# Kernel tuning notes

Hardware: AMD Instinct MI355X
Metric: run time of the kernel (lower is better)

The kernel has to match this reference:

```python
import jax, jax.numpy as jnp
import numpy as np

B, S, D, H, FF = 4, 2048, 512, 8, 2048
HD = D // H
SCALE = float(D) ** 0.5  # original scales by sqrt(embed_dim), not sqrt(head_dim)
EPS = 1e-5


def setup_inputs() -> dict:
    key = jax.random.key(0)
    ks = jax.random.split(key, 16)
    s_in = 1.0 / np.sqrt(D)
    s_ff = 1.0 / np.sqrt(FF)
    return {
        "embeddings": jax.random.normal(ks[0], (B, S, D), dtype=jnp.float32),
        "mask": jnp.ones((B, S), dtype=bool),
        # per-head Q/K/V projections stacked: [H, D, HD]
        "Wq": jax.random.uniform(ks[1], (H, D, HD), jnp.float32, -s_in, s_in),
        "bq": jax.random.uniform(ks[2], (H, HD), jnp.float32, -s_in, s_in),
        "Wk": jax.random.uniform(ks[3], (H, D, HD), jnp.float32, -s_in, s_in),
        "bk": jax.random.uniform(ks[4], (H, HD), jnp.float32, -s_in, s_in),
        "Wv": jax.random.uniform(ks[5], (H, D, HD), jnp.float32, -s_in, s_in),
        "bv": jax.random.uniform(ks[6], (H, HD), jnp.float32, -s_in, s_in),
        "Wc": jax.random.uniform(ks[7], (D, D), jnp.float32, -s_in, s_in),
        "bc": jax.random.uniform(ks[8], (D,), jnp.float32, -s_in, s_in),
        "W1": jax.random.uniform(ks[9], (D, FF), jnp.float32, -s_in, s_in),
        "b1": jax.random.uniform(ks[10], (FF,), jnp.float32, -s_in, s_in),
        "W2": jax.random.uniform(ks[11], (FF, D), jnp.float32, -s_ff, s_ff),
        "b2": jax.random.uniform(ks[12], (D,), jnp.float32, -s_ff, s_ff),
        "gamma": jnp.ones((D,), jnp.float32),
        "beta": jnp.zeros((D,), jnp.float32),
    }


def reference(embeddings, mask, Wq, bq, Wk, bk, Wv, bv, Wc, bc, W1, b1, W2, b2, gamma, beta):
    # Per-head projections batched into one einsum each: [B,H,S,HD]
    Q = jnp.einsum("bsd,hdf->bhsf", embeddings, Wq) + bq[:, None, :]
    K = jnp.einsum("bsd,hdf->bhsf", embeddings, Wk) + bk[:, None, :]
    V = jnp.einsum("bsd,hdf->bhsf", embeddings, Wv) + bv[:, None, :]
    # NOTE: the original computes a masked score tensor but then softmaxes the
    # UNMASKED scores (bug). We faithfully ignore the mask here.
    scores = jnp.einsum("bhsf,bhtf->bhst", Q, K) / SCALE  # [B,H,S,S]
    A = jax.nn.softmax(scores, axis=-1)
    Hh = jnp.einsum("bhst,bhtf->bhsf", A, V)  # [B,H,S,HD]
    # concat heads along feature dim (head h -> contiguous slice)
    Hcat = jnp.transpose(Hh, (0, 2, 1, 3)).reshape(B, S, D)
    Hp = Hcat @ Wc + bc
    # add & norm (dropout is identity at eval)
    res = Hp + embeddings
    mu = jnp.mean(res, axis=-1, keepdims=True)
    var = jnp.var(res, axis=-1, keepdims=True)
    Hn = (res - mu) / jnp.sqrt(var + EPS) * gamma + beta
    out = jax.nn.relu(Hn @ W1 + b1) @ W2 + b2  # no residual after FFN in original
    return out, mask
```

## Files before the change

### kernel.cpp

```cpp
#include <hip/hip_runtime.h>
#include <hip/hip_bf16.h>
#include <cstdint>
#include <cstddef>

typedef short  s16x8 __attribute__((ext_vector_type(8)));
typedef short  s16x4 __attribute__((ext_vector_type(4)));
typedef float  f32x4 __attribute__((ext_vector_type(4)));
typedef unsigned u32x2 __attribute__((ext_vector_type(2)));

static constexpr int Bb = 4, Ss = 2048, Dd = 512, Hh = 8, HDd = 64, FFf = 2048;
static constexpr int Mm = Bb * Ss;

__device__ __forceinline__ unsigned short f2bf(float f) {
  unsigned u = __float_as_uint(f);
  u += 0x7FFFu + ((u >> 16) & 1u);
  return (unsigned short)(u >> 16);
}

__device__ __forceinline__ unsigned cvt_pk_bf16(float lo, float hi) {
  unsigned r;
  asm("v_cvt_pk_bf16_f32 %0, %1, %2" : "=v"(r) : "v"(lo), "v"(hi));
  return r;
}

__device__ __forceinline__ float exp2_raw(float x) {
  float r;
  asm("v_exp_f32 %0, %1\n\ts_nop 0" : "=v"(r) : "v"(x));
  return r;
}

#define GLOAD_LDS16(gp, lp)                                                     \
  __builtin_amdgcn_global_load_lds((const __attribute__((address_space(1))) void*)(gp), \
                                   (__attribute__((address_space(3))) void*)(lp), 16, 0, 0)

__device__ __forceinline__ void xpose_tile(const float* __restrict__ in,
                                           unsigned short* __restrict__ out,
                                           int K, int N, int bx, int by, float (*t)[33]) {
  const int lx = threadIdx.x & 31, ly = threadIdx.x >> 5;
  const int n0 = bx * 32, k0 = by * 32;
#pragma unroll
  for (int r = 0; r < 4; ++r) t[ly + r * 8][lx] = in[(size_t)(k0 + ly + r * 8) * N + n0 + lx];
  __syncthreads();
#pragma unroll
  for (int r = 0; r < 4; ++r)
    out[(size_t)(n0 + ly + r * 8) * K + k0 + lx] = f2bf(t[lx][ly + r * 8]);
}

__global__ __launch_bounds__(256) void prep_all(
    const float* __restrict__ emb, const float* __restrict__ Wq, const float* __restrict__ Wk,
    const float* __restrict__ Wv, const float* __restrict__ Wc, const float* __restrict__ W1,
    const float* __restrict__ W2, unsigned short* __restrict__ embB,
    unsigned short* __restrict__ WtQKV, unsigned short* __restrict__ WtC,
    unsigned short* __restrict__ Wt1, unsigned short* __restrict__ Wt2,
    float* __restrict__ maskOut) {
  __shared__ float t[32][33];
  const int blk = blockIdx.x;
  if (blk < 4096) {
    const int i = blk * 256 + threadIdx.x;
    const float4 v = reinterpret_cast<const float4*>(emb)[i];
    s16x4 o; o[0] = f2bf(v.x); o[1] = f2bf(v.y); o[2] = f2bf(v.z); o[3] = f2bf(v.w);
    reinterpret_cast<s16x4*>(embB)[i] = o;
  } else if (blk < 4864) {
    const int b = blk - 4096;
    const int bx = b & 15, by = (b >> 4) & 1, z = b >> 5;
    const int sel = z >> 3, h = z & 7;
    const float* W = sel == 0 ? Wq : (sel == 1 ? Wk : Wv);
    const float* inb = W + (size_t)h * 512 * 64;
    unsigned short* outb = WtQKV + (size_t)sel * 512 * 512 + (size_t)h * 64 * 512;
    const int lx = threadIdx.x & 31, ly = threadIdx.x >> 5;
    const int d0 = bx * 32, f0 = by * 32;
#pragma unroll
    for (int r = 0; r < 4; ++r) t[ly + r * 8][lx] = inb[(size_t)(d0 + ly + r * 8) * 64 + f0 + lx];
    __syncthreads();
#pragma unroll
    for (int r = 0; r < 4; ++r)
      outb[(size_t)(f0 + ly + r * 8) * 512 + d0 + lx] = f2bf(t[lx][ly + r * 8]);
  } else if (blk < 5120) {
    const int b = blk - 4864;
    xpose_tile(Wc, WtC, 512, 512, b & 15, b >> 4, t);
  } else if (blk < 6144) {
    const int b = blk - 5120;
    xpose_tile(W1, Wt1, 512, 2048, b & 63, b >> 6, t);
  } else if (blk < 7168) {
    const int b = blk - 6144;
    xpose_tile(W2, Wt2, 2048, 512, b & 15, b >> 4, t);
  } else {
    const int i = (blk - 7168) * 256 + threadIdx.x;
    if (i < Bb * Ss) maskOut[i] = 1.0f;
  }
}

__global__ __launch_bounds__(256) void vtrans(const unsigned short* __restrict__ Vn,
                                              unsigned short* __restrict__ Vt) {
  __shared__ unsigned short t[64][72];
  const int bh = blockIdx.y, s0 = blockIdx.x * 64;
  const int row = threadIdx.x >> 2, cs = (threadIdx.x & 3) << 4;
  const unsigned short* src = Vn + (((size_t)bh * 2048 + s0 + row) << 6) + cs;
  *reinterpret_cast<s16x8*>(&t[row][cs]) = *reinterpret_cast<const s16x8*>(src);
  *reinterpret_cast<s16x8*>(&t[row][cs + 8]) = *reinterpret_cast<const s16x8*>(src + 8);
  __syncthreads();
  unsigned ow[8];
#pragma unroll
  for (int j = 0; j < 8; ++j)
    ow[j] = (unsigned)t[cs + 2 * j][row] | ((unsigned)t[cs + 2 * j + 1][row] << 16);
  unsigned short* dst = Vt + (((size_t)bh * 64 + row) << 11) + s0 + cs;
  *reinterpret_cast<uint4*>(dst) = *reinterpret_cast<const uint4*>(&ow[0]);
  *reinterpret_cast<uint4*>(dst + 8) = *reinterpret_cast<const uint4*>(&ow[4]);
}

template<int EPI, int NI>
__global__ __launch_bounds__(256) void gemm_bt(
    const unsigned short* __restrict__ A, const unsigned short* __restrict__ Bt,
    const float* __restrict__ bias0, const float* __restrict__ bias1, const float* __restrict__ bias2,
    const float* __restrict__ addf, float* __restrict__ outF,
    unsigned short* __restrict__ outB0, unsigned short* __restrict__ outB1,
    unsigned short* __restrict__ outB2, int M, int N, int K) {
  constexpr int BN = NI * 32;
  __shared__ alignas(16) unsigned short As[3][128 * 32];
  __shared__ alignas(16) unsigned short Bs[3][BN * 32];
  const int tid = threadIdx.x;
  const int lane = tid & 63, wid = tid >> 6;
  const int wr = wid >> 1, wc = wid & 1;
  const int fr = lane & 15, kg = lane >> 4;
  const int m0 = blockIdx.y * 128, n0 = blockIdx.x * BN;

  const int srow = tid >> 2;
  const int schunk = (tid & 3) ^ ((tid >> 3) & 3);
  const unsigned short* gA = A + (size_t)(m0 + srow) * K + (schunk << 3);
  const unsigned short* gB = Bt + (size_t)(n0 + srow) * K + (schunk << 3);

  auto STAGE = [&](int kt, int buf) {
    unsigned short* lA = &As[buf][wid * 512];
    unsigned short* lB = &Bs[buf][wid * 512];
    GLOAD_LDS16(gA + kt, lA);
    GLOAD_LDS16(gA + (size_t)64 * K + kt, lA + 2048);
    GLOAD_LDS16(gB + kt, lB);
    if constexpr (NI == 4) GLOAD_LDS16(gB + (size_t)64 * K + kt, lB + 2048);
  };

  f32x4 acc[4][NI];
#pragma unroll
  for (int i = 0; i < 4; ++i)
#pragma unroll
    for (int j = 0; j < NI; ++j)
#pragma unroll
      for (int r = 0; r < 4; ++r) acc[i][j][r] = 0.f;

  STAGE(0, 0);
  STAGE(32, 1);
  const int nk = K >> 5;
  int cur = 0;
  const int rchunk = (kg ^ ((fr >> 1) & 3)) << 3;
  for (int ki = 0; ki < nk; ++ki) {
    const int pre = cur == 0 ? 2 : cur - 1;
    __builtin_amdgcn_s_barrier();
    if (ki + 2 < nk) {
      STAGE((ki + 2) << 5, pre);
      if constexpr (NI == 4)
        asm volatile("s_waitcnt vmcnt(8)" ::: "memory");
      else
        asm volatile("s_waitcnt vmcnt(6)" ::: "memory");
    } else if (ki + 1 < nk) {
      if constexpr (NI == 4)
        asm volatile("s_waitcnt vmcnt(4)" ::: "memory");
      else
        asm volatile("s_waitcnt vmcnt(3)" ::: "memory");
    } else {
      asm volatile("s_waitcnt vmcnt(0)" ::: "memory");
    }
    __builtin_amdgcn_sched_barrier(0);
    __builtin_amdgcn_s_barrier();
    __builtin_amdgcn_sched_barrier(0);

    s16x8 af[4], bfv[NI];
#pragma unroll
    for (int i = 0; i < 4; ++i)
      af[i] = *reinterpret_cast<const s16x8*>(&As[cur][(wr * 64 + i * 16 + fr) * 32 + rchunk]);
#pragma unroll
    for (int i = 0; i < NI; ++i)
      bfv[i] = *reinterpret_cast<const s16x8*>(
          &Bs[cur][(wc * (NI * 16) + i * 16 + fr) * 32 + rchunk]);
    __builtin_amdgcn_s_setprio(1);
#pragma unroll
    for (int mi = 0; mi < 4; ++mi)
#pragma unroll
      for (int ni = 0; ni < NI; ++ni)
        acc[mi][ni] = __builtin_amdgcn_mfma_f32_16x16x32_bf16(af[mi], bfv[ni], acc[mi][ni], 0, 0, 0);
    __builtin_amdgcn_s_setprio(0);
    cur = cur == 2 ? 0 : cur + 1;
  }

#pragma unroll
  for (int mi = 0; mi < 4; ++mi)
#pragma unroll
    for (int ni = 0; ni < NI; ++ni)
#pragma unroll
      for (int r = 0; r < 4; ++r) {
        const int row = m0 + wr * 64 + mi * 16 + kg * 4 + r;
        const int col = n0 + wc * (NI * 16) + ni * 16 + fr;
        float v = acc[mi][ni][r];
        if constexpr (EPI == 0) {
          const int sel = col >> 9, c = col & 511;
          const float* bs = sel == 0 ? bias0 : (sel == 1 ? bias1 : bias2);
          v += bs[c];
          const int b = row >> 11, s = row & 2047;
          const int h = c >> 6, f = c & 63;
          unsigned short* ob = sel == 0 ? outB0 : (sel == 1 ? outB1 : outB2);
          ob[((size_t)((b << 3) + h) * 2048 + s) * 64 + f] = f2bf(v);
        } else if constexpr (EPI == 1) {
          const size_t idx = (size_t)row * 512 + col;
          outF[idx] = v + bias0[col] + addf[idx];
        } else if constexpr (EPI == 2) {
          v += bias0[col];
          outB0[(size_t)row * 2048 + col] = f2bf(v > 0.f ? v : 0.f);
        } else {
          outF[(size_t)row * 512 + col] = v + bias0[col];
        }
      }
}

__global__ __launch_bounds__(256) void attn_kernel(const unsigned short* __restrict__ Q,
                                                   const unsigned short* __restrict__ Kx,
                                                   const unsigned short* __restrict__ V,
                                                   unsigned short* __restrict__ Hcat) {
  const int lane = threadIdx.x & 63, wid = threadIdx.x >> 6;
  const int fr = lane & 15, kg = lane >> 4;
  const int lin = blockIdx.x;
  const int xcd = lin & 7, idx = lin >> 3;
  const int bh = xcd * 4 + (idx & 3);
  const int qi = idx >> 2;
  const int b = bh >> 3, h = bh & 7;
  const int q0 = qi * 64 + wid * 16;
  const unsigned short* Qh = Q + (size_t)bh * Ss * HDd;
  const unsigned short* Kh = Kx + (size_t)bh * Ss * HDd;
  const unsigned short* Vh = V + (size_t)bh * HDd * Ss;

  __shared__ alignas(16) unsigned short Ks[2][64 * 64];
  __shared__ alignas(16) unsigned short Vs[64 * 64];
  __shared__ alignas(16) unsigned short P[4][16][72];

  const int srow = lane >> 3;
  const int scol = ((lane & 7) ^ srow) << 3;
  const unsigned short* gK0 = Kh + (size_t)(8 * (2 * wid + 0) + srow) * 64 + scol;
  const unsigned short* gK1 = Kh + (size_t)(8 * (2 * wid + 1) + srow) * 64 + scol;
  const unsigned short* gV0 = Vh + (size_t)(8 * (2 * wid + 0) + srow) * 2048 + scol;
  const unsigned short* gV1 = Vh + (size_t)(8 * (2 * wid + 1) + srow) * 2048 + scol;
  unsigned short* lK0a = &Ks[0][(2 * wid + 0) * 512];
  unsigned short* lK1a = &Ks[0][(2 * wid + 1) * 512];
  unsigned short* lK0b = &Ks[1][(2 * wid + 0) * 512];
  unsigned short* lK1b = &Ks[1][(2 * wid + 1) * 512];
  unsigned short* lV0 = &Vs[(2 * wid + 0) * 512];
  unsigned short* lV1 = &Vs[(2 * wid + 1) * 512];

  s16x8 bq[2];
#pragma unroll
  for (int kb = 0; kb < 2; ++kb)
    bq[kb] = *reinterpret_cast<const s16x8*>(&Qh[(size_t)(q0 + fr) * 64 + kb * 32 + kg * 8]);

  f32x4 o[4];
#pragma unroll
  for (int ct = 0; ct < 4; ++ct)
#pragma unroll
    for (int r = 0; r < 4; ++r) o[ct][r] = 0.f;
  float mr = -1e30f, lsum = 0.f;

  const float iscL = 1.4426950408889634f * 0.044194173824159216f;
  const int swz = (fr & 7) << 3;

  GLOAD_LDS16(gK0, lK0a);
  GLOAD_LDS16(gK1, lK1a);
  GLOAD_LDS16(gV0, lV0);
  GLOAD_LDS16(gV1, lV1);

#pragma unroll 1
  for (int t = 0; t < 32; ++t) {
    const int kt = t * 64;
    const int ktn = (kt + 64) & 2047;
    const unsigned short* KsC = Ks[t & 1];
    unsigned short* nK0 = (t & 1) ? lK0a : lK0b;
    unsigned short* nK1 = (t & 1) ? lK1a : lK1b;

    asm volatile("s_waitcnt vmcnt(2)" ::: "memory");
    __builtin_amdgcn_sched_barrier(0);
    __builtin_amdgcn_s_barrier();
    __builtin_amdgcn_sched_barrier(0);

    f32x4 sc[4];
#pragma unroll
    for (int ct = 0; ct < 4; ++ct)
#pragma unroll
      for (int r = 0; r < 4; ++r) sc[ct][r] = 0.f;
    __builtin_amdgcn_s_setprio(1);
#pragma unroll
    for (int ct = 0; ct < 4; ++ct)
#pragma unroll
      for (int kb = 0; kb < 2; ++kb) {
        const s16x8 kf = *reinterpret_cast<const s16x8*>(
            &KsC[(ct * 16 + fr) * 64 + (((kg << 3) + (kb << 5)) ^ swz)]);
        sc[ct] = __builtin_amdgcn_mfma_f32_16x16x32_bf16(kf, bq[kb], sc[ct], 0, 0, 0);
      }
    __builtin_amdgcn_s_setprio(0);

    GLOAD_LDS16(gK0 + (size_t)ktn * 64, nK0);
    GLOAD_LDS16(gK1 + (size_t)ktn * 64, nK1);

    float mxl;
    {
      const float a0 = fmaxf(fmaxf(sc[0][0], sc[0][1]), fmaxf(sc[0][2], sc[0][3]));
      const float a1 = fmaxf(fmaxf(sc[1][0], sc[1][1]), fmaxf(sc[1][2], sc[1][3]));
      const float a2 = fmaxf(fmaxf(sc[2][0], sc[2][1]), fmaxf(sc[2][2], sc[2][3]));
      const float a3 = fmaxf(fmaxf(sc[3][0], sc[3][1]), fmaxf(sc[3][2], sc[3][3]));
      mxl = fmaxf(fmaxf(a0, a1), fmaxf(a2, a3)) * iscL;
    }
    if (!__all(mxl <= mr + 8.0f)) {
      float mx = fmaxf(mxl, __shfl_xor(mxl, 16));
      mx = fmaxf(mx, __shfl_xor(mx, 32));
      const float mn = fmaxf(mr, mx);
      const float corr = exp2_raw(mr - mn);
      mr = mn;
      lsum *= corr;
      float corrq[4];
#pragma unroll
      for (int r = 0; r < 4; ++r) corrq[r] = __shfl(corr, kg * 4 + r);
#pragma unroll
      for (int ct = 0; ct < 4; ++ct)
#pragma unroll
        for (int r = 0; r < 4; ++r) o[ct][r] *= corrq[r];
    }

    float ps0 = 0.f, ps1 = 0.f;
#pragma unroll
    for (int ct = 0; ct < 4; ++ct) {
      float p0 = exp2_raw(__builtin_fmaf(sc[ct][0], iscL, -mr));
      float p1 = exp2_raw(__builtin_fmaf(sc[ct][1], iscL, -mr));
      float p2 = exp2_raw(__builtin_fmaf(sc[ct][2], iscL, -mr));
      float p3 = exp2_raw(__builtin_fmaf(sc[ct][3], iscL, -mr));
      ps0 += (p0 + p1);
      ps1 += (p2 + p3);
      u32x2 pk;
      pk[0] = cvt_pk_bf16(p0, p1);
      pk[1] = cvt_pk_bf16(p2, p3);
      *reinterpret_cast<u32x2*>(&P[wid][fr][ct * 16 + kg * 4]) = pk;
    }
    lsum += ps0 + ps1;

    asm volatile("s_waitcnt vmcnt(2)" ::: "memory");
    __builtin_amdgcn_sched_barrier(0);
    __builtin_amdgcn_s_barrier();
    __builtin_amdgcn_sched_barrier(0);

    const s16x8 pa0 = *reinterpret_cast<const s16x8*>(&P[wid][fr][kg * 8]);
    const s16x8 pa1 = *reinterpret_cast<const s16x8*>(&P[wid][fr][32 + kg * 8]);
    __builtin_amdgcn_s_setprio(1);
#pragma unroll
    for (int ct = 0; ct < 4; ++ct) {
      const s16x8 bv0 = *reinterpret_cast<const s16x8*>(
          &Vs[(ct * 16 + fr) * 64 + (((kg << 3) + 0) ^ swz)]);
      o[ct] = __builtin_amdgcn_mfma_f32_16x16x32_bf16(pa0, bv0, o[ct], 0, 0, 0);
      const s16x8 bv1 = *reinterpret_cast<const s16x8*>(
          &Vs[(ct * 16 + fr) * 64 + (((kg << 3) + 32) ^ swz)]);
      o[ct] = __builtin_amdgcn_mfma_f32_16x16x32_bf16(pa1, bv1, o[ct], 0, 0, 0);
    }
    __builtin_amdgcn_s_setprio(0);

    __builtin_amdgcn_s_barrier();
    __builtin_amdgcn_sched_barrier(0);
    GLOAD_LDS16(gV0 + ktn, lV0);
    GLOAD_LDS16(gV1 + ktn, lV1);
  }

  lsum += __shfl_xor(lsum, 16);
  lsum += __shfl_xor(lsum, 32);
  float invq[4];
#pragma unroll
  for (int r = 0; r < 4; ++r) invq[r] = 1.0f / __shfl(lsum, kg * 4 + r);
#pragma unroll
  for (int ct = 0; ct < 4; ++ct)
#pragma unroll
    for (int r = 0; r < 4; ++r) {
      const int qrow = q0 + kg * 4 + r;
      Hcat[(size_t)(b * Ss + qrow) * Dd + h * 64 + ct * 16 + fr] = f2bf(o[ct][r] * invq[r]);
    }
}

__global__ __launch_bounds__(256) void layernorm_k(const float* __restrict__ res,
                                                   const float* __restrict__ gamma,
                                                   const float* __restrict__ beta,
                                                   unsigned short* __restrict__ out) {
  const int lane = threadIdx.x & 63, wid = threadIdx.x >> 6;
  const int row = blockIdx.x * 4 + wid;
  const float* rp = res + (size_t)row * 512 + lane * 8;
  const float4 v0 = *reinterpret_cast<const float4*>(rp);
  const float4 v1 = *reinterpret_cast<const float4*>(rp + 4);
  float x[8] = {v0.x, v0.y, v0.z, v0.w, v1.x, v1.y, v1.z, v1.w};
  float s = 0.f, q = 0.f;
#pragma unroll
  for (int j = 0; j < 8; ++j) { s += x[j]; q += x[j] * x[j]; }
#pragma unroll
  for (int off = 32; off; off >>= 1) { s += __shfl_xor(s, off); q += __shfl_xor(q, off); }
  const float mean = s * (1.f / 512.f);
  const float var = q * (1.f / 512.f) - mean * mean;
  const float rstd = rsqrtf(var + 1e-5f);
  s16x8 o;
#pragma unroll
  for (int j = 0; j < 8; ++j) {
    const int c = lane * 8 + j;
    o[j] = f2bf((x[j] - mean) * rstd * gamma[c] + beta[c]);
  }
  *reinterpret_cast<s16x8*>(out + (size_t)row * 512 + lane * 8) = o;
}

extern "C" void kernel_launch(void* const* d_in, const int* in_sizes, int n_in,
                              void* d_out, int out_size, void* d_ws, size_t ws_size,
                              hipStream_t stream) {
  const float* emb = (const float*)d_in[0];
  const float* Wq = (const float*)d_in[2];
  const float* bq = (const float*)d_in[3];
  const float* Wk = (const float*)d_in[4];
  const float* bk = (const float*)d_in[5];
  const float* Wv = (const float*)d_in[6];
  const float* bv = (const float*)d_in[7];
  const float* Wc = (const float*)d_in[8];
  const float* bc = (const float*)d_in[9];
  const float* W1 = (const float*)d_in[10];
  const float* b1 = (const float*)d_in[11];
  const float* W2 = (const float*)d_in[12];
  const float* b2 = (const float*)d_in[13];
  const float* gamma = (const float*)d_in[14];
  const float* beta = (const float*)d_in[15];
  float* out = (float*)d_out;

  char* ws = (char*)d_ws;
  size_t off = 0;
  auto alloc = [&](size_t bytes) {
    char* p = ws + off;
    off = (off + bytes + 255) & ~(size_t)255;
    return p;
  };
  unsigned short* embB = (unsigned short*)alloc((size_t)Mm * Dd * 2);
  unsigned short* WtQKV = (unsigned short*)alloc((size_t)1536 * 512 * 2);
  unsigned short* WtC = (unsigned short*)alloc((size_t)512 * 512 * 2);
  unsigned short* Wt1 = (unsigned short*)alloc((size_t)2048 * 512 * 2);
  unsigned short* Wt2 = (unsigned short*)alloc((size_t)512 * 2048 * 2);
  unsigned short* Qb = (unsigned short*)alloc((size_t)Mm * Dd * 2);
  unsigned short* Kb = (unsigned short*)alloc((size_t)Mm * Dd * 2);
  unsigned short* Vt = (unsigned short*)alloc((size_t)Mm * Dd * 2);
  unsigned short* Hcat = (unsigned short*)alloc((size_t)Mm * Dd * 2);
  float* resF = (float*)alloc((size_t)Mm * Dd * 4);
  unsigned short* HnB = (unsigned short*)alloc((size_t)Mm * Dd * 2);
  unsigned short* G = Qb;
  unsigned short* Vn = HnB;

  prep_all<<<7200, 256, 0, stream>>>(emb, Wq, Wk, Wv, Wc, W1, W2,
                                     embB, WtQKV, WtC, Wt1, Wt2,
                                     out + (size_t)Mm * Dd);

  gemm_bt<0, 4><<<dim3(12, 64), 256, 0, stream>>>(embB, WtQKV, bq, bk, bv, nullptr, nullptr,
                                                  Qb, Kb, Vn, Mm, 1536, 512);
  vtrans<<<dim3(32, 32), 256, 0, stream>>>(Vn, Vt);
  attn_kernel<<<1024, 256, 0, stream>>>(Qb, Kb, Vt, Hcat);
  gemm_bt<1, 2><<<dim3(8, 64), 256, 0, stream>>>(Hcat, WtC, bc, nullptr, nullptr, emb, resF,
                                                 nullptr, nullptr, nullptr, Mm, 512, 512);
  layernorm_k<<<2048, 256, 0, stream>>>(resF, gamma, beta, HnB);
  gemm_bt<2, 4><<<dim3(16, 64), 256, 0, stream>>>(HnB, Wt1, b1, nullptr, nullptr, nullptr, nullptr,
                                                  G, nullptr, nullptr, Mm, 2048, 512);
  gemm_bt<3, 2><<<dim3(8, 64), 256, 0, stream>>>(G, Wt2, b2, nullptr, nullptr, nullptr, out,
                                                 nullptr, nullptr, nullptr, Mm, 512, 2048);
}
```

Measured before the change: 186.4 us.

## Double-buffer V tile and collapse attention loop to one barrier per iteration

The attention kernel now double-buffers V in LDS as well as K. All four global-to-LDS prefetches for the next tile are issued right after a single barrier at the top of each iteration, which drops the two extra block barriers that previously guarded V reuse and the P exchange. The aim is to cut synchronisation stalls and give the V loads a full iteration to land. In exchange, LDS use per block grows by 8 KB, which may lower the number of resident blocks per CU.

```diff
diff --git a/kernel.cpp b/kernel.cpp
--- a/kernel.cpp
+++ b/kernel.cpp
@@ -236,7 +236,7 @@
   const unsigned short* Vh = V + (size_t)bh * HDd * Ss;
 
   __shared__ alignas(16) unsigned short Ks[2][64 * 64];
-  __shared__ alignas(16) unsigned short Vs[64 * 64];
+  __shared__ alignas(16) unsigned short Vs[2][64 * 64];
   __shared__ alignas(16) unsigned short P[4][16][72];
 
   const int srow = lane >> 3;
@@ -245,12 +245,7 @@
   const unsigned short* gK1 = Kh + (size_t)(8 * (2 * wid + 1) + srow) * 64 + scol;
   const unsigned short* gV0 = Vh + (size_t)(8 * (2 * wid + 0) + srow) * 2048 + scol;
   const unsigned short* gV1 = Vh + (size_t)(8 * (2 * wid + 1) + srow) * 2048 + scol;
-  unsigned short* lK0a = &Ks[0][(2 * wid + 0) * 512];
-  unsigned short* lK1a = &Ks[0][(2 * wid + 1) * 512];
-  unsigned short* lK0b = &Ks[1][(2 * wid + 0) * 512];
-  unsigned short* lK1b = &Ks[1][(2 * wid + 1) * 512];
-  unsigned short* lV0 = &Vs[(2 * wid + 0) * 512];
-  unsigned short* lV1 = &Vs[(2 * wid + 1) * 512];
+  const int lds0 = (2 * wid + 0) * 512, lds1 = (2 * wid + 1) * 512;
 
   s16x8 bq[2];
 #pragma unroll
@@ -267,24 +262,26 @@
   const float iscL = 1.4426950408889634f * 0.044194173824159216f;
   const int swz = (fr & 7) << 3;
 
-  GLOAD_LDS16(gK0, lK0a);
-  GLOAD_LDS16(gK1, lK1a);
-  GLOAD_LDS16(gV0, lV0);
-  GLOAD_LDS16(gV1, lV1);
+  GLOAD_LDS16(gK0, &Ks[0][lds0]);
+  GLOAD_LDS16(gK1, &Ks[0][lds1]);
+  GLOAD_LDS16(gV0, &Vs[0][lds0]);
+  GLOAD_LDS16(gV1, &Vs[0][lds1]);
 
 #pragma unroll 1
   for (int t = 0; t < 32; ++t) {
-    const int kt = t * 64;
-    const int ktn = (kt + 64) & 2047;
-    const unsigned short* KsC = Ks[t & 1];
-    unsigned short* nK0 = (t & 1) ? lK0a : lK0b;
-    unsigned short* nK1 = (t & 1) ? lK1a : lK1b;
-
-    asm volatile("s_waitcnt vmcnt(2)" ::: "memory");
+    const int cur = t & 1;
+    const int ktn = (t * 64 + 64) & 2047;
+
+    asm volatile("s_waitcnt vmcnt(0)" ::: "memory");
     __builtin_amdgcn_sched_barrier(0);
     __builtin_amdgcn_s_barrier();
     __builtin_amdgcn_sched_barrier(0);
 
+    GLOAD_LDS16(gK0 + (size_t)ktn * 64, &Ks[cur ^ 1][lds0]);
+    GLOAD_LDS16(gK1 + (size_t)ktn * 64, &Ks[cur ^ 1][lds1]);
+    GLOAD_LDS16(gV0 + ktn, &Vs[cur ^ 1][lds0]);
+    GLOAD_LDS16(gV1 + ktn, &Vs[cur ^ 1][lds1]);
+
     f32x4 sc[4];
 #pragma unroll
     for (int ct = 0; ct < 4; ++ct)
@@ -296,13 +293,10 @@
 #pragma unroll
       for (int kb = 0; kb < 2; ++kb) {
         const s16x8 kf = *reinterpret_cast<const s16x8*>(
-            &KsC[(ct * 16 + fr) * 64 + (((kg << 3) + (kb << 5)) ^ swz)]);
+            &Ks[cur][(ct * 16 + fr) * 64 + (((kg << 3) + (kb << 5)) ^ swz)]);
         sc[ct] = __builtin_amdgcn_mfma_f32_16x16x32_bf16(kf, bq[kb], sc[ct], 0, 0, 0);
       }
     __builtin_amdgcn_s_setprio(0);
-
-    GLOAD_LDS16(gK0 + (size_t)ktn * 64, nK0);
-    GLOAD_LDS16(gK1 + (size_t)ktn * 64, nK1);
 
     float mxl;
     {
@@ -344,29 +338,19 @@
     }
     lsum += ps0 + ps1;
 
-    asm volatile("s_waitcnt vmcnt(2)" ::: "memory");
-    __builtin_amdgcn_sched_barrier(0);
-    __builtin_amdgcn_s_barrier();
-    __builtin_amdgcn_sched_barrier(0);
-
     const s16x8 pa0 = *reinterpret_cast<const s16x8*>(&P[wid][fr][kg * 8]);
     const s16x8 pa1 = *reinterpret_cast<const s16x8*>(&P[wid][fr][32 + kg * 8]);
     __builtin_amdgcn_s_setprio(1);
 #pragma unroll
     for (int ct = 0; ct < 4; ++ct) {
       const s16x8 bv0 = *reinterpret_cast<const s16x8*>(
-          &Vs[(ct * 16 + fr) * 64 + (((kg << 3) + 0) ^ swz)]);
+          &Vs[cur][(ct * 16 + fr) * 64 + (((kg << 3) + 0) ^ swz)]);
       o[ct] = __builtin_amdgcn_mfma_f32_16x16x32_bf16(pa0, bv0, o[ct], 0, 0, 0);
       const s16x8 bv1 = *reinterpret_cast<const s16x8*>(
-          &Vs[(ct * 16 + fr) * 64 + (((kg << 3) + 32) ^ swz)]);
+          &Vs[cur][(ct * 16 + fr) * 64 + (((kg << 3) + 32) ^ swz)]);
       o[ct] = __builtin_amdgcn_mfma_f32_16x16x32_bf16(pa1, bv1, o[ct], 0, 0, 0);
     }
     __builtin_amdgcn_s_setprio(0);
-
-    __builtin_amdgcn_s_barrier();
-    __builtin_amdgcn_sched_barrier(0);
-    GLOAD_LDS16(gV0 + ktn, lV0);
-    GLOAD_LDS16(gV1 + ktn, lV1);
   }
 
   lsum += __shfl_xor(lsum, 16);
```

Measured after the change: 216.2 us. 1.16x slower.
